# Performance work log

Hardware: AMD Instinct MI355X
Metric: run time of the kernel (lower is better)

Reference implementation:

```python
import jax, jax.numpy as jnp
import numpy as np

D_MODEL = 1024
H = 16
D_HEAD = 64  # d_q = d_k = d_v
B = 2
S = 2048


def setup_inputs() -> dict:
    key = jax.random.key(0)
    ks = jax.random.split(key, 12)
    scale = 1.0 / np.sqrt(D_MODEL)
    inp = {
        "q": jax.random.normal(ks[0], (B, S, D_MODEL), dtype=jnp.float32),
        "k": jax.random.normal(ks[1], (B, S, D_MODEL), dtype=jnp.float32),
        "v": jax.random.normal(ks[2], (B, S, D_MODEL), dtype=jnp.float32),
        "mask": jax.random.uniform(ks[3], (S, S), dtype=jnp.float32),
        # stacked per-head projection weights: [H, d_model, d_head]
        "W_q": jax.random.normal(ks[4], (H, D_MODEL, D_HEAD), dtype=jnp.float32) * scale,
        "b_q": jnp.zeros((H, D_HEAD), dtype=jnp.float32),
        "W_k": jax.random.normal(ks[5], (H, D_MODEL, D_HEAD), dtype=jnp.float32) * scale,
        "b_k": jnp.zeros((H, D_HEAD), dtype=jnp.float32),
        "W_v": jax.random.normal(ks[6], (H, D_MODEL, D_HEAD), dtype=jnp.float32) * scale,
        "b_v": jnp.zeros((H, D_HEAD), dtype=jnp.float32),
        # output projection: [H*d_v, d_model]
        "W_o": jax.random.normal(ks[7], (H * D_HEAD, D_MODEL), dtype=jnp.float32) * (1.0 / np.sqrt(H * D_HEAD)),
        "b_o": jnp.zeros((D_MODEL,), dtype=jnp.float32),
    }
    return inp


def reference(q, k, v, mask, W_q, b_q, W_k, b_k, W_v, b_v, W_o, b_o):
    # Batched QKV projections over all heads (original loops per head).
    Q = jnp.einsum("bsd,hde->bhse", q, W_q) + b_q[None, :, None, :]  # [B,H,S,Dh]
    K = jnp.einsum("bsd,hde->bhse", k, W_k) + b_k[None, :, None, :]
    V = jnp.einsum("bsd,hde->bhse", v, W_v) + b_v[None, :, None, :]
    scale = 1.0 / jnp.sqrt(jnp.asarray(D_HEAD, dtype=Q.dtype))
    # NOTE: mask is MULTIPLICATIVE on the scaled scores (as in the original).
    scores = jnp.einsum("bhse,bhte->bhst", Q, K) * scale * mask  # [B,H,S,S]
    attn = jax.nn.softmax(scores, axis=-1)
    heads = jnp.einsum("bhst,bhte->bhse", attn, V)  # [B,H,S,Dh]
    # concat heads along feature dim (head order matches torch cat order)
    concat = jnp.transpose(heads, (0, 2, 1, 3)).reshape(B, S, H * D_HEAD)
    return concat @ W_o + b_o
```

## Files before the change

kernel.cpp:

```cpp
#include <hip/hip_runtime.h>
#include <stdint.h>

#define DM 1024
#define HNUM 16
#define DH 64
#define BB 2
#define SSEQ 2048

typedef unsigned short ushort_t;
typedef __attribute__((ext_vector_type(8))) short bf16x8;
typedef __attribute__((ext_vector_type(4))) float f32x4;
typedef __attribute__((ext_vector_type(16))) float f32x16;

#define SCALE2 0.18033688011112042f
#define DEFER_THR 11.0f

__device__ __forceinline__ ushort_t f2bf(float f) {
  unsigned u = __builtin_bit_cast(unsigned, f);
  u += 0x7FFFu + ((u >> 16) & 1u);
  return (ushort_t)(u >> 16);
}
__device__ __forceinline__ float bf2f(ushort_t h) {
  return __builtin_bit_cast(float, (unsigned)h << 16);
}
__device__ __forceinline__ float fast_exp2(float x) {
#if __has_builtin(__builtin_amdgcn_exp2f)
  return __builtin_amdgcn_exp2f(x);
#else
  return exp2f(x);
#endif
}
__device__ __forceinline__ unsigned cvt_pk_bf16(float lo, float hi) {
  unsigned r;
  asm("v_cvt_pk_bf16_f32 %0, %1, %2" : "=v"(r) : "v"(lo), "v"(hi));
  return r;
}
__device__ __forceinline__ void plane32_swap(unsigned& a, unsigned& b, int hh) {
#if __has_builtin(__builtin_amdgcn_permlane32_swap)
  typedef int v2i __attribute__((ext_vector_type(2)));
  v2i r = __builtin_amdgcn_permlane32_swap((int)a, (int)b, 0, 0);
  a = (unsigned)r.x; b = (unsigned)r.y;
#else
  unsigned sa = (unsigned)__shfl_xor((int)a, 32);
  unsigned sb = (unsigned)__shfl_xor((int)b, 32);
  unsigned na = hh ? sb : a;
  unsigned nb = hh ? b : sa;
  a = na; b = nb;
#endif
}

typedef const __attribute__((address_space(1))) unsigned int* gas_ptr;
typedef __attribute__((address_space(3))) unsigned int* las_ptr;
__device__ __forceinline__ void gload_lds16(const void* g, void* l) {
  __builtin_amdgcn_global_load_lds((gas_ptr)(uintptr_t)g, (las_ptr)(uintptr_t)l, 16, 0, 0);
}

__global__ void prep_all(const float* __restrict__ q, const float* __restrict__ k,
                         const float* __restrict__ v, const float* __restrict__ mask,
                         const float* __restrict__ Wq, const float* __restrict__ Wk,
                         const float* __restrict__ Wv, const float* __restrict__ Wo,
                         ushort_t* __restrict__ qd, ushort_t* __restrict__ kd,
                         ushort_t* __restrict__ vd, ushort_t* __restrict__ maskd,
                         ushort_t* __restrict__ dq, ushort_t* __restrict__ dk,
                         ushort_t* __restrict__ dv, ushort_t* __restrict__ dWo) {
  __shared__ ushort_t T[64][65];
  const int bx = blockIdx.x, tid = threadIdx.x;
  if (bx < 6144) {
    const int z = bx >> 11, bi = bx & 2047;
    const float* src = z == 0 ? q : (z == 1 ? k : v);
    ushort_t* dst    = z == 0 ? qd : (z == 1 ? kd : vd);
    const int idx = bi * 256 + tid;
    const float4* s4 = (const float4*)src;
    float4 a = s4[idx * 2], c = s4[idx * 2 + 1];
    union { ushort_t h[8]; uint4 u; } o;
    o.h[0] = f2bf(a.x); o.h[1] = f2bf(a.y); o.h[2] = f2bf(a.z); o.h[3] = f2bf(a.w);
    o.h[4] = f2bf(c.x); o.h[5] = f2bf(c.y); o.h[6] = f2bf(c.z); o.h[7] = f2bf(c.w);
    ((uint4*)dst)[idx] = o.u;
  } else if (bx < 8192) {
    const int TG = bx - 6144;
    const int Tt = TG >> 6, G = TG & 63;
    #pragma unroll
    for (int i = 0; i < 2; ++i) {
      const int wd = tid * 2 + i;
      const int l = wd & 63, g2 = (wd >> 6) & 3, a = wd >> 8;
      const int qr = G * 32 + (l & 31);
      const int t = Tt * 64 + a * 32 + g2 * 8 + (l >> 5) * 4;
      float4 mv = *(const float4*)(mask + (size_t)qr * 2048 + t);
      union { ushort_t h4[4]; uint2 u; } pk;
      pk.h4[0] = f2bf(mv.x * SCALE2); pk.h4[1] = f2bf(mv.y * SCALE2);
      pk.h4[2] = f2bf(mv.z * SCALE2); pk.h4[3] = f2bf(mv.w * SCALE2);
      *(uint2*)(maskd + (size_t)TG * 2048 + (size_t)wd * 4) = pk.u;
    }
  } else if (bx < 8960) {
    const int id = bx - 8192;
    const int zz = id >> 4, yy = id & 15;
    const int mat = zz >> 4, g = zz & 15;
    const float* src = (mat == 0 ? Wq : (mat == 1 ? Wk : Wv)) + (size_t)g * 1024 * 64;
    ushort_t* dst    = (mat == 0 ? dq : (mat == 1 ? dk : dv)) + (size_t)g * 1024 * 64;
    const int r0 = yy * 64;
    #pragma unroll
    for (int i = 0; i < 16; ++i) {
      int idx = i * 256 + tid;
      int r = idx >> 6, c = idx & 63;
      T[r][c] = f2bf(src[(size_t)(r0 + r) * 64 + c]);
    }
    __syncthreads();
    #pragma unroll
    for (int i = 0; i < 16; ++i) {
      int idx = i * 256 + tid;
      int cc = idx >> 6, rr = idx & 63;
      dst[(size_t)cc * 1024 + r0 + rr] = T[rr][cc];
    }
  } else {
    const int id = bx - 8960;
    const int c0 = (id & 15) * 64, r0 = (id >> 4) * 64;
    #pragma unroll
    for (int i = 0; i < 16; ++i) {
      int idx = i * 256 + tid;
      int r = idx >> 6, c = idx & 63;
      T[r][c] = f2bf(Wo[(size_t)(r0 + r) * 1024 + c0 + c]);
    }
    __syncthreads();
    #pragma unroll
    for (int i = 0; i < 16; ++i) {
      int idx = i * 256 + tid;
      int cc = idx >> 6, rr = idx & 63;
      dWo[(size_t)(c0 + cc) * 1024 + r0 + rr] = T[rr][cc];
    }
  }
}

__device__ __forceinline__ void gemm_mainloop_128(const ushort_t* __restrict__ A,
                                                  const ushort_t* __restrict__ Bm,
                                                  f32x4 (&acc)[4][4], int m0, int n0, int l, int w) {
  __shared__ ushort_t As[128 * 64];
  __shared__ ushort_t Bs[128 * 64];
  const int wr = w >> 1, wc = w & 1;
  for (int ks = 0; ks < 16; ++ks) {
    const int k0 = ks * 64;
    #pragma unroll
    for (int it = 0; it < 4; ++it) {
      const int chunk = it * 4 + w;
      const int row = chunk * 8 + (l >> 3);
      const int kc = ((l & 7) * 8) ^ ((row & 7) * 8);
      gload_lds16(A + (size_t)(m0 + row) * 1024 + k0 + kc, (char*)As + chunk * 1024);
      gload_lds16(Bm + (size_t)(n0 + row) * 1024 + k0 + kc, (char*)Bs + chunk * 1024);
    }
    __syncthreads();
    #pragma unroll
    for (int kk = 0; kk < 2; ++kk) {
      bf16x8 af[4], bfr[4];
      #pragma unroll
      for (int mi = 0; mi < 4; ++mi) {
        const int row = wr * 64 + mi * 16 + (l & 15);
        const int kc = (kk * 32 + (l >> 4) * 8) ^ ((row & 7) * 8);
        af[mi] = *(const bf16x8*)(As + row * 64 + kc);
      }
      #pragma unroll
      for (int ni = 0; ni < 4; ++ni) {
        const int row = wc * 64 + ni * 16 + (l & 15);
        const int kc = (kk * 32 + (l >> 4) * 8) ^ ((row & 7) * 8);
        bfr[ni] = *(const bf16x8*)(Bs + row * 64 + kc);
      }
      #pragma unroll
      for (int mi = 0; mi < 4; ++mi)
        #pragma unroll
        for (int ni = 0; ni < 4; ++ni)
          acc[mi][ni] = __builtin_amdgcn_mfma_f32_16x16x32_bf16(af[mi], bfr[ni], acc[mi][ni], 0, 0, 0);
    }
    __syncthreads();
  }
}

__global__ __launch_bounds__(256, 2) void qkv_gemm(
    const ushort_t* __restrict__ qb, const ushort_t* __restrict__ kb, const ushort_t* __restrict__ vb,
    const ushort_t* __restrict__ Wtq, const ushort_t* __restrict__ Wtk, const ushort_t* __restrict__ Wtv,
    const float* __restrict__ bq, const float* __restrict__ bk, const float* __restrict__ bv,
    ushort_t* __restrict__ Qo, ushort_t* __restrict__ Ko, ushort_t* __restrict__ Vto) {
  const int z = blockIdx.z;
  const ushort_t* A  = z == 0 ? qb : (z == 1 ? kb : vb);
  const ushort_t* Bm = z == 0 ? Wtq : (z == 1 ? Wtk : Wtv);
  const float* bias  = z == 0 ? bq : (z == 1 ? bk : bv);
  ushort_t* out      = z == 0 ? Qo : (z == 1 ? Ko : Vto);
  const int m0 = blockIdx.x * 128, n0 = blockIdx.y * 128;
  const int tid = threadIdx.x, l = tid & 63, w = tid >> 6;
  f32x4 acc[4][4] = {};
  gemm_mainloop_128(A, Bm, acc, m0, n0, l, w);
  const int wr = w >> 1, wc = w & 1;
  #pragma unroll
  for (int mi = 0; mi < 4; ++mi) {
    #pragma unroll
    for (int ni = 0; ni < 4; ++ni) {
      const int n = n0 + wc * 64 + ni * 16 + (l & 15);
      const float bb = bias[n];
      const int mbase = m0 + wr * 64 + mi * 16 + ((l >> 4) << 2);
      if (z < 2) {
        #pragma unroll
        for (int i = 0; i < 4; ++i) {
          const int m = mbase + i;
          const size_t o = (((size_t)((m >> 11) * 16 + (n >> 6))) * 2048 + (m & 2047)) * 64 + (n & 63);
          out[o] = f2bf(acc[mi][ni][i] + bb);
        }
      } else {
        union { ushort_t h[4]; uint2 u2; } pk;
        #pragma unroll
        for (int i = 0; i < 4; ++i) pk.h[i] = f2bf(acc[mi][ni][i] + bb);
        const size_t o = (((size_t)((mbase >> 11) * 16 + (n >> 6))) * 64 + (n & 63)) * 2048 + (mbase & 2047);
        *(uint2*)(out + o) = pk.u2;
      }
    }
  }
}

__global__ __launch_bounds__(256, 2) void out_gemm(const ushort_t* __restrict__ A,
                                                   const ushort_t* __restrict__ Bm,
                                                   const float* __restrict__ bias,
                                                   float* __restrict__ out) {
  __shared__ ushort_t As[64 * 64];
  __shared__ ushort_t Bs[128 * 64];
  const int m0 = blockIdx.x * 64, n0 = blockIdx.y * 128;
  const int tid = threadIdx.x, l = tid & 63, w = tid >> 6;
  const int wr = w >> 1, wc = w & 1;
  f32x4 acc[2][4] = {};
  for (int ks = 0; ks < 16; ++ks) {
    const int k0 = ks * 64;
    #pragma unroll
    for (int it = 0; it < 6; ++it) {
      const int chunk = it * 4 + w;
      if (chunk < 8) {
        const int row = chunk * 8 + (l >> 3);
        const int kc = ((l & 7) * 8) ^ ((row & 7) * 8);
        gload_lds16(A + (size_t)(m0 + row) * 1024 + k0 + kc, (char*)As + chunk * 1024);
      } else {
        const int c2 = chunk - 8;
        const int row = c2 * 8 + (l >> 3);
        const int kc = ((l & 7) * 8) ^ ((row & 7) * 8);
        gload_lds16(Bm + (size_t)(n0 + row) * 1024 + k0 + kc, (char*)Bs + c2 * 1024);
      }
    }
    __syncthreads();
    #pragma unroll
    for (int kk = 0; kk < 2; ++kk) {
      bf16x8 af[2], bfr[4];
      #pragma unroll
      for (int mi = 0; mi < 2; ++mi) {
        const int row = wr * 32 + mi * 16 + (l & 15);
        const int kc = (kk * 32 + (l >> 4) * 8) ^ ((row & 7) * 8);
        af[mi] = *(const bf16x8*)(As + row * 64 + kc);
      }
      #pragma unroll
      for (int ni = 0; ni < 4; ++ni) {
        const int row = wc * 64 + ni * 16 + (l & 15);
        const int kc = (kk * 32 + (l >> 4) * 8) ^ ((row & 7) * 8);
        bfr[ni] = *(const bf16x8*)(Bs + row * 64 + kc);
      }
      #pragma unroll
      for (int mi = 0; mi < 2; ++mi)
        #pragma unroll
        for (int ni = 0; ni < 4; ++ni)
          acc[mi][ni] = __builtin_amdgcn_mfma_f32_16x16x32_bf16(af[mi], bfr[ni], acc[mi][ni], 0, 0, 0);
    }
    __syncthreads();
  }
  #pragma unroll
  for (int mi = 0; mi < 2; ++mi) {
    #pragma unroll
    for (int ni = 0; ni < 4; ++ni) {
      const int n = n0 + wc * 64 + ni * 16 + (l & 15);
      const float bb = bias[n];
      const int mbase = m0 + wr * 32 + mi * 16 + ((l >> 4) << 2);
      #pragma unroll
      for (int i = 0; i < 4; ++i)
        out[(size_t)(mbase + i) * 1024 + n] = acc[mi][ni][i] + bb;
    }
  }
}

__device__ __forceinline__ void stage_kv(const ushort_t* __restrict__ Kb, const ushort_t* __restrict__ Vb,
                                         int t0, ushort_t* ks, ushort_t* vs, int l, int w) {
  #pragma unroll
  for (int half = 0; half < 2; ++half) {
    const int c = half * 4 + w;
    const int r1 = c * 8 + (l >> 3);
    const int cc = ((l & 7) * 8) ^ ((r1 & 7) * 8);
    gload_lds16(Kb + (size_t)(t0 + r1) * 64 + cc, (char*)ks + c * 1024);
    gload_lds16(Vb + (size_t)r1 * 2048 + t0 + cc, (char*)vs + c * 1024);
  }
}

__global__ __launch_bounds__(256, 2) void flash_attn(const ushort_t* __restrict__ Q,
                                                     const ushort_t* __restrict__ K,
                                                     const ushort_t* __restrict__ Vt,
                                                     const ushort_t* __restrict__ maskF,
                                                     ushort_t* __restrict__ concat) {
  const int bh = blockIdx.y, b = bh >> 4, h = bh & 15;
  const int tid = threadIdx.x, l = tid & 63, w = tid >> 6;
  const int hh = l >> 5, q_l = l & 31;
  __shared__ ushort_t Ks[2][64 * 64];
  __shared__ ushort_t Vs[2][64 * 64];
  const ushort_t* Qb = Q + (size_t)bh * 2048 * 64;
  const ushort_t* Kb = K + (size_t)bh * 2048 * 64;
  const ushort_t* Vb = Vt + (size_t)bh * 64 * 2048;
  const int qbase = blockIdx.x * 128 + w * 32;
  const int G = qbase >> 5;

  bf16x8 qf[4];
  #pragma unroll
  for (int s = 0; s < 4; ++s)
    qf[s] = *(const bf16x8*)(Qb + (size_t)(qbase + q_l) * 64 + s * 16 + hh * 8);

  float m_run = -1e30f, l_run = 0.f;
  f32x16 po[2] = {};

  stage_kv(Kb, Vb, 0, Ks[0], Vs[0], l, w);
  int cur = 0;

  for (int t0 = 0; t0 < 2048; t0 += 64) {
    __syncthreads();
    if (t0 + 64 < 2048) stage_kv(Kb, Vb, t0 + 64, Ks[cur ^ 1], Vs[cur ^ 1], l, w);

    const ushort_t* mbase = maskF + (size_t)((t0 >> 6) * 64 + G) * 2048;
    uint2 mw[2][4];
    #pragma unroll
    for (int a = 0; a < 2; ++a)
      #pragma unroll
      for (int g2 = 0; g2 < 4; ++g2)
        mw[a][g2] = *(const uint2*)(mbase + (size_t)(((a * 4 + g2) * 64) + l) * 4);

    f32x16 sc[2] = {};
    #pragma unroll
    for (int s = 0; s < 4; ++s) {
      #pragma unroll
      for (int mt = 0; mt < 2; ++mt) {
        const int row = mt * 32 + q_l;
        const int col = (s * 16 + hh * 8) ^ ((q_l & 7) * 8);
        const bf16x8 kf = *(const bf16x8*)(Ks[cur] + row * 64 + col);
        sc[mt] = __builtin_amdgcn_mfma_f32_32x32x16_bf16(kf, qf[s], sc[mt], 0, 0, 0);
      }
    }

    float tmax = -1e30f;
    #pragma unroll
    for (int a = 0; a < 2; ++a) {
      #pragma unroll
      for (int g2 = 0; g2 < 4; ++g2) {
        const unsigned lo = mw[a][g2].x, hi = mw[a][g2].y;
        float v0 = sc[a][g2 * 4 + 0] * bf2f((ushort_t)lo);
        float v1 = sc[a][g2 * 4 + 1] * bf2f((ushort_t)(lo >> 16));
        float v2 = sc[a][g2 * 4 + 2] * bf2f((ushort_t)hi);
        float v3 = sc[a][g2 * 4 + 3] * bf2f((ushort_t)(hi >> 16));
        sc[a][g2 * 4 + 0] = v0; sc[a][g2 * 4 + 1] = v1;
        sc[a][g2 * 4 + 2] = v2; sc[a][g2 * 4 + 3] = v3;
        tmax = fmaxf(tmax, fmaxf(fmaxf(v0, v1), fmaxf(v2, v3)));
      }
    }
    tmax = fmaxf(tmax, __shfl_xor(tmax, 32));

    if (!__all(tmax <= m_run + DEFER_THR)) {
      const float mnew = fmaxf(m_run, tmax);
      const float rf = fast_exp2(m_run - mnew);
      m_run = mnew;
      l_run *= rf;
      #pragma unroll
      for (int et = 0; et < 2; ++et)
        #pragma unroll
        for (int r = 0; r < 16; ++r) po[et][r] *= rf;
    }

    float psum = 0.f;
    unsigned pw[2][8];
    #pragma unroll
    for (int a = 0; a < 2; ++a)
      #pragma unroll
      for (int j = 0; j < 8; ++j) {
        const float p0 = fast_exp2(sc[a][2 * j] - m_run);
        const float p1 = fast_exp2(sc[a][2 * j + 1] - m_run);
        psum += p0 + p1;
        pw[a][j] = cvt_pk_bf16(p0, p1);
      }
    psum += __shfl_xor(psum, 32);
    l_run += psum;

    #pragma unroll
    for (int a = 0; a < 2; ++a) {
      plane32_swap(pw[a][0], pw[a][2], hh);
      plane32_swap(pw[a][1], pw[a][3], hh);
      plane32_swap(pw[a][4], pw[a][6], hh);
      plane32_swap(pw[a][5], pw[a][7], hh);
    }

    #pragma unroll
    for (int s = 0; s < 4; ++s) {
      union { unsigned u[4]; bf16x8 v; } pf;
      pf.u[0] = pw[s >> 1][(s & 1) * 4 + 0];
      pf.u[1] = pw[s >> 1][(s & 1) * 4 + 1];
      pf.u[2] = pw[s >> 1][(s & 1) * 4 + 2];
      pf.u[3] = pw[s >> 1][(s & 1) * 4 + 3];
      #pragma unroll
      for (int et = 0; et < 2; ++et) {
        const int row = et * 32 + q_l;
        const int col = (s * 16 + hh * 8) ^ ((q_l & 7) * 8);
        const bf16x8 vf = *(const bf16x8*)(Vs[cur] + row * 64 + col);
        po[et] = __builtin_amdgcn_mfma_f32_32x32x16_bf16(vf, pf.v, po[et], 0, 0, 0);
      }
    }
    cur ^= 1;
  }

  const float invl = 1.0f / l_run;
  __syncthreads();
  ushort_t* ow = &Ks[0][0] + w * 2048;
  #pragma unroll
  for (int et = 0; et < 2; ++et)
    #pragma unroll
    for (int r = 0; r < 16; ++r) {
      const int e = et * 32 + (r & 3) + 8 * (r >> 2) + 4 * hh;
      const int ba = (q_l * 128 + e * 2) ^ ((q_l & 7) << 4);
      *(ushort_t*)((char*)ow + ba) = f2bf(po[et][r] * invl);
    }
  __syncthreads();
  {
    union { ushort_t hs[32]; uint2 u2[8]; uint4 u4[4]; } ov;
    const int ebase = hh * 32;
    #pragma unroll
    for (int c = 0; c < 8; ++c) {
      const int e0 = ebase + c * 4;
      const int ba = (q_l * 128 + e0 * 2) ^ ((q_l & 7) << 4);
      ov.u2[c] = *(const uint2*)((const char*)ow + ba);
    }
    ushort_t* dst = concat + ((size_t)(b * 2048 + qbase + q_l)) * 1024 + h * 64 + ebase;
    #pragma unroll
    for (int c2 = 0; c2 < 4; ++c2)
      ((uint4*)dst)[c2] = ov.u4[c2];
  }
}

extern "C" void kernel_launch(void* const* d_in, const int* in_sizes, int n_in,
                              void* d_out, int out_size, void* d_ws, size_t ws_size,
                              hipStream_t stream) {
  const float* q    = (const float*)d_in[0];
  const float* k    = (const float*)d_in[1];
  const float* v    = (const float*)d_in[2];
  const float* mask = (const float*)d_in[3];
  const float* Wq   = (const float*)d_in[4];
  const float* bq   = (const float*)d_in[5];
  const float* Wk   = (const float*)d_in[6];
  const float* bk   = (const float*)d_in[7];
  const float* Wv   = (const float*)d_in[8];
  const float* bv   = (const float*)d_in[9];
  const float* Wo   = (const float*)d_in[10];
  const float* bo   = (const float*)d_in[11];

  const size_t SZ8M = (size_t)4096 * 1024 * 2;
  const size_t SZ2M = (size_t)1024 * 1024 * 2;
  if (ws_size < 7 * SZ8M + 4 * SZ2M) return;

  char* p = (char*)d_ws;
  ushort_t* qb    = (ushort_t*)p; p += SZ8M;
  ushort_t* kb    = (ushort_t*)p; p += SZ8M;
  ushort_t* vb    = (ushort_t*)p; p += SZ8M;
  ushort_t* maskb = (ushort_t*)p; p += SZ8M;
  ushort_t* Qo    = (ushort_t*)p; p += SZ8M;
  ushort_t* Ko    = (ushort_t*)p; p += SZ8M;
  ushort_t* Vto   = (ushort_t*)p; p += SZ8M;
  ushort_t* Wtq   = (ushort_t*)p; p += SZ2M;
  ushort_t* Wtk   = (ushort_t*)p; p += SZ2M;
  ushort_t* Wtv   = (ushort_t*)p; p += SZ2M;
  ushort_t* Wot   = (ushort_t*)p; p += SZ2M;
  ushort_t* concat = qb;

  prep_all<<<dim3(9216), dim3(256), 0, stream>>>(q, k, v, mask, Wq, Wk, Wv, Wo,
                                                 qb, kb, vb, maskb, Wtq, Wtk, Wtv, Wot);
  qkv_gemm<<<dim3(32, 8, 3), dim3(256), 0, stream>>>(qb, kb, vb, Wtq, Wtk, Wtv, bq, bk, bv, Qo, Ko, Vto);
  flash_attn<<<dim3(16, 32), dim3(256), 0, stream>>>(Qo, Ko, Vto, maskb, concat);
  out_gemm<<<dim3(64, 8), dim3(256), 0, stream>>>(concat, Wot, bo, (float*)d_out);
}
```

Before: 135.0 us.

## Split attention over key halves and merge partials in a combine kernel

The flash attention grid gains a key-split dimension, so each block handles half of the key sequence and writes a normalized partial output plus its running max and sum. A new combine kernel rescales and sums the two partials into the concat buffer before the output GEMM. The grid grows from 512 to 1024 blocks, and the launch bound now targets 4 blocks per SM, to fill the GPU better. The cost is an extra kernel launch, extra memory traffic for the two partial buffers, and an added bf16 rounding step on the partials.

```diff
diff --git a/kernel.cpp b/kernel.cpp
--- a/kernel.cpp
+++ b/kernel.cpp
@@ -288,12 +288,15 @@
   }
 }
 
-__global__ __launch_bounds__(256, 2) void flash_attn(const ushort_t* __restrict__ Q,
+__global__ __launch_bounds__(256, 4) void flash_attn(const ushort_t* __restrict__ Q,
                                                      const ushort_t* __restrict__ K,
                                                      const ushort_t* __restrict__ Vt,
                                                      const ushort_t* __restrict__ maskF,
-                                                     ushort_t* __restrict__ concat) {
+                                                     ushort_t* __restrict__ part0,
+                                                     ushort_t* __restrict__ part1,
+                                                     float2* __restrict__ mlp) {
   const int bh = blockIdx.y, b = bh >> 4, h = bh & 15;
+  const int h2 = blockIdx.z;
   const int tid = threadIdx.x, l = tid & 63, w = tid >> 6;
   const int hh = l >> 5, q_l = l & 31;
   __shared__ ushort_t Ks[2][64 * 64];
@@ -303,6 +306,7 @@
   const ushort_t* Vb = Vt + (size_t)bh * 64 * 2048;
   const int qbase = blockIdx.x * 128 + w * 32;
   const int G = qbase >> 5;
+  const int tbase = h2 * 1024;
 
   bf16x8 qf[4];
   #pragma unroll
@@ -312,12 +316,13 @@
   float m_run = -1e30f, l_run = 0.f;
   f32x16 po[2] = {};
 
-  stage_kv(Kb, Vb, 0, Ks[0], Vs[0], l, w);
+  stage_kv(Kb, Vb, tbase, Ks[0], Vs[0], l, w);
   int cur = 0;
 
-  for (int t0 = 0; t0 < 2048; t0 += 64) {
-    __syncthreads();
-    if (t0 + 64 < 2048) stage_kv(Kb, Vb, t0 + 64, Ks[cur ^ 1], Vs[cur ^ 1], l, w);
+  for (int tt = 0; tt < 16; ++tt) {
+    const int t0 = tbase + tt * 64;
+    __syncthreads();
+    if (tt + 1 < 16) stage_kv(Kb, Vb, t0 + 64, Ks[cur ^ 1], Vs[cur ^ 1], l, w);
 
     const ushort_t* mbase = maskF + (size_t)((t0 >> 6) * 64 + G) * 2048;
     uint2 mw[2][4];
@@ -407,6 +412,10 @@
     cur ^= 1;
   }
 
+  if (hh == 0)
+    mlp[(size_t)(h2 * 32 + bh) * 2048 + qbase + q_l] = make_float2(m_run, l_run);
+
+  ushort_t* outp = h2 ? part1 : part0;
   const float invl = 1.0f / l_run;
   __syncthreads();
   ushort_t* ow = &Ks[0][0] + w * 2048;
@@ -428,11 +437,34 @@
       const int ba = (q_l * 128 + e0 * 2) ^ ((q_l & 7) << 4);
       ov.u2[c] = *(const uint2*)((const char*)ow + ba);
     }
-    ushort_t* dst = concat + ((size_t)(b * 2048 + qbase + q_l)) * 1024 + h * 64 + ebase;
+    ushort_t* dst = outp + ((size_t)(b * 2048 + qbase + q_l)) * 1024 + h * 64 + ebase;
     #pragma unroll
     for (int c2 = 0; c2 < 4; ++c2)
       ((uint4*)dst)[c2] = ov.u4[c2];
   }
+}
+
+__global__ void combine(const ushort_t* __restrict__ p0, const ushort_t* __restrict__ p1,
+                        const float2* __restrict__ mlp, ushort_t* __restrict__ outc) {
+  const int idx = blockIdx.x * 256 + threadIdx.x;
+  const int flat = idx * 8;
+  const int row = flat >> 10, col = flat & 1023;
+  const int b = row >> 11, s = row & 2047, h = col >> 6;
+  const int bh = b * 16 + h;
+  const float2 a = mlp[(size_t)bh * 2048 + s];
+  const float2 c = mlp[(size_t)(32 + bh) * 2048 + s];
+  const float M = fmaxf(a.x, c.x);
+  float w1 = fast_exp2(a.x - M) * a.y;
+  float w2 = fast_exp2(c.x - M) * c.y;
+  const float inv = 1.0f / (w1 + w2);
+  w1 *= inv; w2 *= inv;
+  union { uint4 u; ushort_t h8[8]; } u0, u1, o;
+  u0.u = ((const uint4*)p0)[idx];
+  u1.u = ((const uint4*)p1)[idx];
+  #pragma unroll
+  for (int j = 0; j < 8; ++j)
+    o.h8[j] = f2bf(w1 * bf2f(u0.h8[j]) + w2 * bf2f(u1.h8[j]));
+  ((uint4*)outc)[idx] = o.u;
 }
 
 extern "C" void kernel_launch(void* const* d_in, const int* in_sizes, int n_in,
@@ -468,10 +500,14 @@
   ushort_t* Wtv   = (ushort_t*)p; p += SZ2M;
   ushort_t* Wot   = (ushort_t*)p; p += SZ2M;
   ushort_t* concat = qb;
+  ushort_t* part0 = kb;
+  ushort_t* part1 = vb;
+  float2*   mlbuf = (float2*)Wtq;
 
   prep_all<<<dim3(9216), dim3(256), 0, stream>>>(q, k, v, mask, Wq, Wk, Wv, Wo,
                                                  qb, kb, vb, maskb, Wtq, Wtk, Wtv, Wot);
   qkv_gemm<<<dim3(32, 8, 3), dim3(256), 0, stream>>>(qb, kb, vb, Wtq, Wtk, Wtv, bq, bk, bv, Qo, Ko, Vto);
-  flash_attn<<<dim3(16, 32), dim3(256), 0, stream>>>(Qo, Ko, Vto, maskb, concat);
+  flash_attn<<<dim3(16, 32, 2), dim3(256), 0, stream>>>(Qo, Ko, Vto, maskb, part0, part1, mlbuf);
+  combine<<<dim3(2048), dim3(256), 0, stream>>>(part0, part1, mlbuf, concat);
   out_gemm<<<dim3(64, 8), dim3(256), 0, stream>>>(concat, Wot, bo, (float*)d_out);
 }
```

Measured after the change: 138.0 us. 2.2% more time.
